# Kernel tuning notes

Measured on AMD Instinct MI355X. Metric: run time of the kernel, lower is better.

## Reference

```python
import jax, jax.numpy as jnp
import numpy as np

N_LEAVES = 262144  # 2^18, perfect binary tree
INPUT_SIZE = 64
HIDDEN = 128


def setup_inputs() -> dict:
    key = jax.random.key(0)
    ks = jax.random.split(key, 7)
    s_in = 1.0 / np.sqrt(INPUT_SIZE)
    s_h = 1.0 / np.sqrt(HIDDEN)
    return {
        "leaf_x": jax.random.normal(ks[0], (N_LEAVES, INPUT_SIZE), dtype=jnp.float32),
        "W_in": jax.random.uniform(ks[1], (INPUT_SIZE, HIDDEN), jnp.float32, -s_in, s_in),
        "b_in": jax.random.uniform(ks[2], (HIDDEN,), jnp.float32, -s_in, s_in),
        "W_l": jax.random.uniform(ks[3], (HIDDEN, HIDDEN), jnp.float32, -s_h, s_h),
        "b_l": jax.random.uniform(ks[4], (HIDDEN,), jnp.float32, -s_h, s_h),
        "W_r": jax.random.uniform(ks[5], (HIDDEN, HIDDEN), jnp.float32, -s_h, s_h),
        "b_r": jax.random.uniform(ks[6], (HIDDEN,), jnp.float32, -s_h, s_h),
    }


def reference(leaf_x, W_in, b_in, W_l, b_l, W_r, b_r):
    # Leaf rule: h = tanh(input2h(x))  -- batched over all leaves at once.
    h = jnp.tanh(leaf_x @ W_in + b_in)  # [N_LEAVES, HIDDEN]
    # Internal rule: h = tanh(left_h(l) + right_h(r)); note torch adds BOTH
    # linear biases, i.e. b_l + b_r. Perfect binary tree -> batch each depth
    # level as one GEMM pair. Python loop over log2(N) static levels only.
    n = h.shape[0]
    depth = int(np.log2(n))
    for _ in range(depth):
        h = jnp.tanh(h[0::2] @ W_l + h[1::2] @ W_r + (b_l + b_r))
    return h  # root hidden state, shape [1, HIDDEN]
```

## Files before the change

### kernel.cpp

```cpp
#include <hip/hip_runtime.h>
#include <hip/hip_bf16.h>


typedef unsigned short u16;
typedef unsigned int u32;
typedef __attribute__((ext_vector_type(8))) short bf16x8;
typedef __attribute__((ext_vector_type(4))) float f32x4;

#define TANH_S 2.8853900817779268f

__device__ __forceinline__ u16 f2bf(float f) {
    __hip_bfloat16 h = __float2bfloat16(f);
    return *(u16*)&h;
}
__device__ __forceinline__ u32 f2bf_pk(float a, float b) {
    __hip_bfloat162 h = __float22bfloat162_rn(make_float2(a, b));
    return *(u32*)&h;
}
__device__ __forceinline__ float tanh_ps(float xs) {
#if __has_builtin(__builtin_amdgcn_exp2f) && __has_builtin(__builtin_amdgcn_rcpf)
    float t = __builtin_amdgcn_exp2f(xs);
    float r = __builtin_amdgcn_rcpf(t + 1.0f);
    return __builtin_fmaf(-2.0f, r, 1.0f);
#else
    float e = __expf(xs * 0.6931471805599453f);
    return 1.0f - 2.0f / (e + 1.0f);
#endif
}
__device__ __forceinline__ int swz(int row, int c) {
    return c ^ (((row >> 3) & 3) << 3);
}

#define MFMA16(a, b, c) __builtin_amdgcn_mfma_f32_16x16x32_bf16((a), (b), (c), 0, 0, 0)

#define WS_BWIN 32768
#define WS_BYTES 81920

__global__ __launch_bounds__(256) void kprep(
    const float* __restrict__ Win, const float* __restrict__ Wl,
    const float* __restrict__ Wr, u16* __restrict__ ws) {
    const int tid = threadIdx.x;
    const int w = tid >> 6, lane = tid & 63, quad = lane >> 4, lq = lane & 15;
    const int c0 = 32 * w + 2 * lq;
    const int part = blockIdx.x;
    if (part < 4) {
#pragma unroll
        for (int kk = 0; kk < 2; ++kk) {
            const int kc = part * 2 + kk;
            const float* W = (kc < 4) ? Wl : Wr;
            const int kbase = (kc & 3) * 32 + quad * 8;
            bf16x8 f0, f1;
#pragma unroll
            for (int j = 0; j < 8; ++j) {
                float2 v = *(const float2*)(W + (size_t)(kbase + j) * 128 + c0);
                f0[j] = (short)f2bf(v.x * TANH_S);
                f1[j] = (short)f2bf(v.y * TANH_S);
            }
            *(bf16x8*)(ws + (kc * 2 + 0) * 2048 + tid * 8) = f0;
            *(bf16x8*)(ws + (kc * 2 + 1) * 2048 + tid * 8) = f1;
        }
    } else {
#pragma unroll
        for (int kc = 0; kc < 2; ++kc) {
            const int kbase = kc * 32 + quad * 8;
            bf16x8 f0, f1;
#pragma unroll
            for (int j = 0; j < 8; ++j) {
                float2 v = *(const float2*)(Win + (size_t)(kbase + j) * 128 + c0);
                f0[j] = (short)f2bf(v.x * TANH_S);
                f1[j] = (short)f2bf(v.y * TANH_S);
            }
            *(bf16x8*)(ws + WS_BWIN + (kc * 2 + 0) * 2048 + tid * 8) = f0;
            *(bf16x8*)(ws + WS_BWIN + (kc * 2 + 1) * 2048 + tid * 8) = f1;
        }
    }
}

__device__ __forceinline__ void load_bw_ws(const u16* __restrict__ ws, int tid,
                                           bf16x8 (&bw)[8][2]) {
#pragma unroll
    for (int kc = 0; kc < 8; ++kc) {
        bw[kc][0] = *(const bf16x8*)(ws + (kc * 2 + 0) * 2048 + tid * 8);
        bw[kc][1] = *(const bf16x8*)(ws + (kc * 2 + 1) * 2048 + tid * 8);
    }
}

__device__ __forceinline__ void run_levels_mfma(
    u16* b0, u16* b1, int Mfirst, int Mlast, const bf16x8 (&bw)[8][2],
    float bs0, float bs1, float* finalOut, int quad, int lq, int c0) {
    u16* in = b0;
    u16* out = b1;
    for (int M = Mfirst; M >= Mlast; M >>= 1) {
        const int ntiles = (M + 15) >> 4;
        for (int rt = 0; rt < ntiles; ++rt) {
            const int r0e = rt * 16;
            bf16x8 a[8];
#pragma unroll
            for (int kc = 0; kc < 8; ++kc) {
                const int row = 2 * (r0e + lq) + (kc >> 2);
                const int kb = (kc & 3) * 32 + quad * 8;
                a[kc] = *(const bf16x8*)(in + row * 136 + swz(row, kb));
            }
            f32x4 ac0 = {bs0, bs0, bs0, bs0}, ac1 = {bs1, bs1, bs1, bs1};
#pragma unroll
            for (int kc = 0; kc < 8; ++kc) {
                ac0 = MFMA16(a[kc], bw[kc][0], ac0);
                ac1 = MFMA16(a[kc], bw[kc][1], ac1);
            }
#pragma unroll
            for (int r = 0; r < 4; ++r) {
                const int ro = r0e + quad * 4 + r;
                if (ro < M) {
                    float v0 = tanh_ps(ac0[r]);
                    float v1 = tanh_ps(ac1[r]);
                    if (M == Mlast) {
                        *(float2*)(finalOut + ro * 128 + c0) = make_float2(v0, v1);
                    } else {
                        *(u32*)(out + ro * 136 + swz(ro, c0)) = f2bf_pk(v0, v1);
                    }
                }
            }
        }
        __syncthreads();
        u16* t = in; in = out; out = t;
    }
}

__global__ __launch_bounds__(256, 2) void kfront(
    float* XB, const float* __restrict__ bin,
    const float* __restrict__ bl, const float* __restrict__ br,
    const u16* __restrict__ ws) {
    __shared__ __align__(16) u16 H0[128 * 136];
    __shared__ __align__(16) u16 POOL[128 * 72];

    const int tid = threadIdx.x;
    const int w = tid >> 6, lane = tid & 63, quad = lane >> 4, lq = lane & 15;
    const int b = blockIdx.x;
    const int c0 = 32 * w + 2 * lq;
    u16* Xa = POOL;
    u16* H1 = POOL;

    const float* Xg = XB + (size_t)b * 8192;
#pragma unroll
    for (int t = 0; t < 8; ++t) {
        int i4 = tid + 256 * t;
        int r = i4 >> 4, k4 = (i4 & 15) << 2;
        float4 v = *(const float4*)(Xg + r * 64 + k4);
        *(uint2*)(Xa + r * 72 + k4) =
            make_uint2(f2bf_pk(v.x, v.y), f2bf_pk(v.z, v.w));
    }

    bf16x8 bwin[2][2];
#pragma unroll
    for (int kc = 0; kc < 2; ++kc) {
        bwin[kc][0] = *(const bf16x8*)(ws + WS_BWIN + (kc * 2 + 0) * 2048 + tid * 8);
        bwin[kc][1] = *(const bf16x8*)(ws + WS_BWIN + (kc * 2 + 1) * 2048 + tid * 8);
    }
    bf16x8 bw[8][2];
    load_bw_ws(ws, tid, bw);

    const float2 binp = *(const float2*)(bin + c0);
    const float2 blp = *(const float2*)(bl + c0);
    const float2 brp = *(const float2*)(br + c0);
    const float bi0 = binp.x * TANH_S, bi1 = binp.y * TANH_S;
    const float bs0 = (blp.x + brp.x) * TANH_S, bs1 = (blp.y + brp.y) * TANH_S;
    __syncthreads();

    for (int rt = 0; rt < 8; ++rt) {
        const int r0e = rt * 16;
        const int rowa = r0e + lq;
        bf16x8 a0 = *(const bf16x8*)(Xa + rowa * 72 + quad * 8);
        bf16x8 a1 = *(const bf16x8*)(Xa + rowa * 72 + 32 + quad * 8);
        f32x4 ac0 = {bi0, bi0, bi0, bi0}, ac1 = {bi1, bi1, bi1, bi1};
        ac0 = MFMA16(a0, bwin[0][0], ac0);
        ac0 = MFMA16(a1, bwin[1][0], ac0);
        ac1 = MFMA16(a0, bwin[0][1], ac1);
        ac1 = MFMA16(a1, bwin[1][1], ac1);
#pragma unroll
        for (int r = 0; r < 4; ++r) {
            const int ro = r0e + quad * 4 + r;
            *(u32*)(H0 + ro * 136 + swz(ro, c0)) =
                f2bf_pk(tanh_ps(ac0[r]), tanh_ps(ac1[r]));
        }
    }
    __syncthreads();

    run_levels_mfma(H0, H1, 64, 4, bw, bs0, bs1, XB + (size_t)b * 8192,
                    quad, lq, c0);
}

__global__ __launch_bounds__(256) void kmid(
    float* XB, const float* __restrict__ bl, const float* __restrict__ br,
    const u16* __restrict__ ws) {
    __shared__ __align__(16) u16 H0[128 * 136];
    __shared__ __align__(16) u16 H1[64 * 136];

    const int tid = threadIdx.x;
    const int w = tid >> 6, lane = tid & 63, quad = lane >> 4, lq = lane & 15;
    const int t = blockIdx.x;
    const int c0 = 32 * w + 2 * lq;

    bf16x8 bw[8][2];
    load_bw_ws(ws, tid, bw);

#pragma unroll
    for (int it = 0; it < 16; ++it) {
        int i4 = tid + 256 * it;
        int r = i4 >> 5, k4 = (i4 & 31) << 2;
        const float* src = XB + (size_t)8192 * (32 * t + (r >> 2)) + (r & 3) * 128 + k4;
        float4 v = *(const float4*)src;
        *(uint2*)(H0 + r * 136 + swz(r, k4)) =
            make_uint2(f2bf_pk(v.x, v.y), f2bf_pk(v.z, v.w));
    }
    const float2 blp = *(const float2*)(bl + c0);
    const float2 brp = *(const float2*)(br + c0);
    const float bs0 = (blp.x + brp.x) * TANH_S, bs1 = (blp.y + brp.y) * TANH_S;
    __syncthreads();

    run_levels_mfma(H0, H1, 64, 1, bw, bs0, bs1,
                    XB + (size_t)262144 * t + 512, quad, lq, c0);
}

__global__ __launch_bounds__(256) void ktail(
    const float* XB, const float* __restrict__ bl, const float* __restrict__ br,
    const u16* __restrict__ ws, float* __restrict__ out) {
    __shared__ __align__(16) u16 H0[64 * 136];
    __shared__ __align__(16) u16 H1[64 * 136];

    const int tid = threadIdx.x;
    const int w = tid >> 6, lane = tid & 63, quad = lane >> 4, lq = lane & 15;
    const int c0 = 32 * w + 2 * lq;

    bf16x8 bw[8][2];
    load_bw_ws(ws, tid, bw);

#pragma unroll
    for (int it = 0; it < 8; ++it) {
        int i4 = tid + 256 * it;
        int r = i4 >> 5, k4 = (i4 & 31) << 2;
        float4 v = *(const float4*)(XB + (size_t)262144 * r + 512 + k4);
        *(uint2*)(H0 + r * 136 + swz(r, k4)) =
            make_uint2(f2bf_pk(v.x, v.y), f2bf_pk(v.z, v.w));
    }
    const float2 blp = *(const float2*)(bl + c0);
    const float2 brp = *(const float2*)(br + c0);
    const float bs0 = (blp.x + brp.x) * TANH_S, bs1 = (blp.y + brp.y) * TANH_S;
    __syncthreads();

    run_levels_mfma(H0, H1, 32, 1, bw, bs0, bs1, out, quad, lq, c0);
}

extern "C" void kernel_launch(void* const* d_in, const int* in_sizes, int n_in,
                              void* d_out, int out_size, void* d_ws, size_t ws_size,
                              hipStream_t stream) {
    float* XB = (float*)d_in[0];
    const float* Win = (const float*)d_in[1];
    const float* bin = (const float*)d_in[2];
    const float* Wl  = (const float*)d_in[3];
    const float* bl  = (const float*)d_in[4];
    const float* Wr  = (const float*)d_in[5];
    const float* br  = (const float*)d_in[6];
    float* out = (float*)d_out;
    u16* ws = (u16*)d_ws;

    kprep<<<5, 256, 0, stream>>>(Win, Wl, Wr, ws);
    kfront<<<2048, 256, 0, stream>>>(XB, bin, bl, br, ws);
    kmid<<<64, 256, 0, stream>>>(XB, bl, br, ws);
    ktail<<<1, 256, 0, stream>>>(XB, bl, br, ws, out);
}
```

Before: 142.0 us.

## Halve front tiles, store bf16 intermediates in workspace, fuse tail via last-block counter

```diff
diff --git a/kernel.cpp b/kernel.cpp
--- a/kernel.cpp
+++ b/kernel.cpp
@@ -34,15 +34,19 @@
 #define MFMA16(a, b, c) __builtin_amdgcn_mfma_f32_16x16x32_bf16((a), (b), (c), 0, 0, 0)
 
 #define WS_BWIN 32768
-#define WS_BYTES 81920
+#define WS_L1_BYTE 81920
+#define WS_L2_BYTE (WS_L1_BYTE + 4194304)
+#define WS_CNT_BYTE (WS_L2_BYTE + 32768)
+#define WS_NEED (WS_CNT_BYTE + 64)
 
 __global__ __launch_bounds__(256) void kprep(
     const float* __restrict__ Win, const float* __restrict__ Wl,
-    const float* __restrict__ Wr, u16* __restrict__ ws) {
+    const float* __restrict__ Wr, u16* __restrict__ ws, u32* counter) {
     const int tid = threadIdx.x;
     const int w = tid >> 6, lane = tid & 63, quad = lane >> 4, lq = lane & 15;
     const int c0 = 32 * w + 2 * lq;
     const int part = blockIdx.x;
+    if (part == 0 && tid == 0 && counter) *counter = 0;
     if (part < 4) {
 #pragma unroll
         for (int kk = 0; kk < 2; ++kk) {
@@ -85,9 +89,22 @@
     }
 }
 
+__device__ __forceinline__ void gather128(u16* H0, const u16* base, int S4,
+                                          int Sin, int tid) {
+#pragma unroll
+    for (int it = 0; it < 8; ++it) {
+        int i4 = tid + 256 * it;
+        int r = i4 >> 4, c8 = (i4 & 15) << 3;
+        uint4 v = *(const uint4*)(base + (size_t)(r >> 2) * S4 + (r & 3) * Sin + c8);
+        *(uint4*)(H0 + r * 136 + swz(r, c8)) = v;
+    }
+}
+
+template <bool BFOUT>
 __device__ __forceinline__ void run_levels_mfma(
     u16* b0, u16* b1, int Mfirst, int Mlast, const bf16x8 (&bw)[8][2],
-    float bs0, float bs1, float* finalOut, int quad, int lq, int c0) {
+    float bs0, float bs1, u16* outB, int ostr, float* outF,
+    int quad, int lq, int c0) {
     u16* in = b0;
     u16* out = b1;
     for (int M = Mfirst; M >= Mlast; M >>= 1) {
@@ -114,7 +131,11 @@
                     float v0 = tanh_ps(ac0[r]);
                     float v1 = tanh_ps(ac1[r]);
                     if (M == Mlast) {
-                        *(float2*)(finalOut + ro * 128 + c0) = make_float2(v0, v1);
+                        if (BFOUT) {
+                            *(u32*)(outB + ro * ostr + c0) = f2bf_pk(v0, v1);
+                        } else {
+                            *(float2*)(outF + ro * 128 + c0) = make_float2(v0, v1);
+                        }
                     } else {
                         *(u32*)(out + ro * 136 + swz(ro, c0)) = f2bf_pk(v0, v1);
                     }
@@ -126,12 +147,12 @@
     }
 }
 
-__global__ __launch_bounds__(256, 2) void kfront(
-    float* XB, const float* __restrict__ bin,
+__global__ __launch_bounds__(256, 4) void kfront(
+    const float* XB, const float* __restrict__ bin,
     const float* __restrict__ bl, const float* __restrict__ br,
-    const u16* __restrict__ ws) {
-    __shared__ __align__(16) u16 H0[128 * 136];
-    __shared__ __align__(16) u16 POOL[128 * 72];
+    const u16* __restrict__ ws, u16* l1, int bstr) {
+    __shared__ __align__(16) u16 H0[64 * 136];
+    __shared__ __align__(16) u16 POOL[64 * 72];
 
     const int tid = threadIdx.x;
     const int w = tid >> 6, lane = tid & 63, quad = lane >> 4, lq = lane & 15;
@@ -140,9 +161,9 @@
     u16* Xa = POOL;
     u16* H1 = POOL;
 
-    const float* Xg = XB + (size_t)b * 8192;
-#pragma unroll
-    for (int t = 0; t < 8; ++t) {
+    const float* Xg = XB + (size_t)b * 4096;
+#pragma unroll
+    for (int t = 0; t < 4; ++t) {
         int i4 = tid + 256 * t;
         int r = i4 >> 4, k4 = (i4 & 15) << 2;
         float4 v = *(const float4*)(Xg + r * 64 + k4);
@@ -166,7 +187,7 @@
     const float bs0 = (blp.x + brp.x) * TANH_S, bs1 = (blp.y + brp.y) * TANH_S;
     __syncthreads();
 
-    for (int rt = 0; rt < 8; ++rt) {
+    for (int rt = 0; rt < 4; ++rt) {
         const int r0e = rt * 16;
         const int rowa = r0e + lq;
         bf16x8 a0 = *(const bf16x8*)(Xa + rowa * 72 + quad * 8);
@@ -185,15 +206,17 @@
     }
     __syncthreads();
 
-    run_levels_mfma(H0, H1, 64, 4, bw, bs0, bs1, XB + (size_t)b * 8192,
-                    quad, lq, c0);
+    run_levels_mfma<true>(H0, H1, 32, 4, bw, bs0, bs1,
+                          l1 + (size_t)b * bstr, 128, nullptr, quad, lq, c0);
 }
 
 __global__ __launch_bounds__(256) void kmid(
-    float* XB, const float* __restrict__ bl, const float* __restrict__ br,
-    const u16* __restrict__ ws) {
+    const u16* l1, int bstr, const float* __restrict__ bl,
+    const float* __restrict__ br, const u16* __restrict__ ws,
+    u16* l2, int lstr, float* __restrict__ out, u32* counter, int do_tail) {
     __shared__ __align__(16) u16 H0[128 * 136];
     __shared__ __align__(16) u16 H1[64 * 136];
+    __shared__ int amlast;
 
     const int tid = threadIdx.x;
     const int w = tid >> 6, lane = tid & 63, quad = lane >> 4, lq = lane & 15;
@@ -203,28 +226,35 @@
     bf16x8 bw[8][2];
     load_bw_ws(ws, tid, bw);
 
-#pragma unroll
-    for (int it = 0; it < 16; ++it) {
-        int i4 = tid + 256 * it;
-        int r = i4 >> 5, k4 = (i4 & 31) << 2;
-        const float* src = XB + (size_t)8192 * (32 * t + (r >> 2)) + (r & 3) * 128 + k4;
-        float4 v = *(const float4*)src;
-        *(uint2*)(H0 + r * 136 + swz(r, k4)) =
-            make_uint2(f2bf_pk(v.x, v.y), f2bf_pk(v.z, v.w));
-    }
+    gather128(H0, l1 + (size_t)(32 * t) * bstr, bstr, 128, tid);
+
     const float2 blp = *(const float2*)(bl + c0);
     const float2 brp = *(const float2*)(br + c0);
     const float bs0 = (blp.x + brp.x) * TANH_S, bs1 = (blp.y + brp.y) * TANH_S;
     __syncthreads();
 
-    run_levels_mfma(H0, H1, 64, 1, bw, bs0, bs1,
-                    XB + (size_t)262144 * t + 512, quad, lq, c0);
+    run_levels_mfma<true>(H0, H1, 64, 1, bw, bs0, bs1,
+                          l2 + (size_t)t * lstr, 128, nullptr, quad, lq, c0);
+
+    if (!do_tail) return;
+    __threadfence();
+    __syncthreads();
+    if (tid == 0) amlast = (atomicAdd(counter, 1u) == 127u) ? 1 : 0;
+    __syncthreads();
+    if (!amlast) return;
+    __threadfence();
+
+    gather128(H0, l2, 4 * lstr, lstr, tid);
+    __syncthreads();
+    run_levels_mfma<false>(H0, H1, 64, 1, bw, bs0, bs1,
+                           nullptr, 0, out, quad, lq, c0);
 }
 
 __global__ __launch_bounds__(256) void ktail(
-    const float* XB, const float* __restrict__ bl, const float* __restrict__ br,
-    const u16* __restrict__ ws, float* __restrict__ out) {
-    __shared__ __align__(16) u16 H0[64 * 136];
+    const u16* l2, int lstr, const float* __restrict__ bl,
+    const float* __restrict__ br, const u16* __restrict__ ws,
+    float* __restrict__ out) {
+    __shared__ __align__(16) u16 H0[128 * 136];
     __shared__ __align__(16) u16 H1[64 * 136];
 
     const int tid = threadIdx.x;
@@ -233,21 +263,15 @@
 
     bf16x8 bw[8][2];
     load_bw_ws(ws, tid, bw);
-
-#pragma unroll
-    for (int it = 0; it < 8; ++it) {
-        int i4 = tid + 256 * it;
-        int r = i4 >> 5, k4 = (i4 & 31) << 2;
-        float4 v = *(const float4*)(XB + (size_t)262144 * r + 512 + k4);
-        *(uint2*)(H0 + r * 136 + swz(r, k4)) =
-            make_uint2(f2bf_pk(v.x, v.y), f2bf_pk(v.z, v.w));
-    }
+    gather128(H0, l2, 4 * lstr, lstr, tid);
+
     const float2 blp = *(const float2*)(bl + c0);
     const float2 brp = *(const float2*)(br + c0);
     const float bs0 = (blp.x + brp.x) * TANH_S, bs1 = (blp.y + brp.y) * TANH_S;
     __syncthreads();
 
-    run_levels_mfma(H0, H1, 32, 1, bw, bs0, bs1, out, quad, lq, c0);
+    run_levels_mfma<false>(H0, H1, 64, 1, bw, bs0, bs1,
+                           nullptr, 0, out, quad, lq, c0);
 }
 
 extern "C" void kernel_launch(void* const* d_in, const int* in_sizes, int n_in,
@@ -263,8 +287,23 @@
     float* out = (float*)d_out;
     u16* ws = (u16*)d_ws;
 
-    kprep<<<5, 256, 0, stream>>>(Win, Wl, Wr, ws);
-    kfront<<<2048, 256, 0, stream>>>(XB, bin, bl, br, ws);
-    kmid<<<64, 256, 0, stream>>>(XB, bl, br, ws);
-    ktail<<<1, 256, 0, stream>>>(XB, bl, br, ws, out);
-}
+    const bool big = (d_ws != nullptr) && (ws_size >= (size_t)WS_NEED);
+    u16* l1; int bstr; u16* l2; int lstr; u32* counter; int do_tail;
+    if (big) {
+        l1 = (u16*)((char*)d_ws + WS_L1_BYTE); bstr = 512;
+        l2 = (u16*)((char*)d_ws + WS_L2_BYTE); lstr = 128;
+        counter = (u32*)((char*)d_ws + WS_CNT_BYTE);
+        do_tail = 1;
+    } else {
+        l1 = (u16*)XB;        bstr = 8192;
+        l2 = (u16*)XB + 4096; lstr = 8192;
+        counter = nullptr;
+        do_tail = 0;
+    }
+
+    kprep<<<5, 256, 0, stream>>>(Win, Wl, Wr, ws, counter);
+    kfront<<<4096, 256, 0, stream>>>(XB, bin, bl, br, ws, l1, bstr);
+    kmid<<<128, 256, 0, stream>>>(l1, bstr, bl, br, ws, l2, lstr, out, counter, do_tail);
+    if (!do_tail)
+        ktail<<<1, 256, 0, stream>>>(l2, lstr, bl, br, ws, out);
+}
```

Result: slower. 153.2 us (+7.9%).
